# Optimization experiments

Measured on AMD Instinct MI355X. Metric: run time of the kernel, lower is better.

The kernel has to match this reference:

```python
import jax, jax.numpy as jnp
import numpy as np
import math

D_MODEL = 2048
NUM_HEADS = 32
NUM_KV_HEADS = 8
HEAD_DIM = D_MODEL // NUM_HEADS  # 64
BATCH = 2
SEQ = 2048


def setup_inputs() -> dict:
    key = jax.random.key(0)
    ks = jax.random.split(key, 5)
    std_q = math.sqrt(2.0 / (D_MODEL + D_MODEL))
    std_kv = math.sqrt(2.0 / (D_MODEL + NUM_KV_HEADS * HEAD_DIM))
    x = jax.random.normal(ks[0], (BATCH, SEQ, D_MODEL), dtype=jnp.float32)
    Wq = jax.random.normal(ks[1], (D_MODEL, D_MODEL), dtype=jnp.float32) * std_q
    Wk = jax.random.normal(ks[2], (NUM_KV_HEADS * HEAD_DIM, D_MODEL), dtype=jnp.float32) * std_kv
    Wv = jax.random.normal(ks[3], (NUM_KV_HEADS * HEAD_DIM, D_MODEL), dtype=jnp.float32) * std_kv
    Wo = jax.random.normal(ks[4], (D_MODEL, D_MODEL), dtype=jnp.float32) * std_q
    return {"x": x, "Wq": Wq, "Wk": Wk, "Wv": Wv, "Wo": Wo}


def reference(x, Wq, Wk, Wv, Wo):
    B, L, _ = x.shape
    group = NUM_HEADS // NUM_KV_HEADS
    # projections: x @ W.T
    q = (x @ Wq.T).reshape(B, L, NUM_HEADS, HEAD_DIM).transpose(0, 2, 1, 3)      # [B,H,L,D]
    k = (x @ Wk.T).reshape(B, L, NUM_KV_HEADS, HEAD_DIM).transpose(0, 2, 1, 3)   # [B,Hkv,L,D]
    v = (x @ Wv.T).reshape(B, L, NUM_KV_HEADS, HEAD_DIM).transpose(0, 2, 1, 3)
    # expand KV heads (repeat_interleave along head dim)
    k = jnp.repeat(k, group, axis=1)  # [B,H,L,D]
    v = jnp.repeat(v, group, axis=1)
    scale = 1.0 / math.sqrt(HEAD_DIM)
    scores = jnp.einsum("bhld,bhsd->bhls", q, k) * scale  # [B,H,L,S]
    causal_mask = jnp.tril(jnp.ones((L, L), dtype=bool))
    scores = jnp.where(causal_mask[None, None], scores, -jnp.inf)
    weights = jax.nn.softmax(scores, axis=-1)
    out = jnp.einsum("bhls,bhsd->bhld", weights, v)  # [B,H,L,D]
    out = out.transpose(0, 2, 1, 3).reshape(B, L, D_MODEL)
    return out @ Wo.T
```

## Files before the change

### kernel.cpp

```cpp
#include <hip/hip_runtime.h>
#include <stdint.h>


typedef unsigned short u16;
typedef short bf16x8 __attribute__((ext_vector_type(8)));
typedef float f32x4 __attribute__((ext_vector_type(4)));

#define D_MODEL 2048
#define QKV_DIM 3072
#define NUM_HEADS 32
#define HEAD_DIM 64
#define SEQ 2048
#define MTOT 4096

static __device__ __forceinline__ u16 f2bf(float f){
  uint32_t u = __builtin_bit_cast(uint32_t, f);
  u += 0x7FFFu + ((u >> 16) & 1u);
  return (u16)(u >> 16);
}

static __device__ __forceinline__ float exp2_fast(float x){
  float r;
  asm("v_exp_f32 %0, %1" : "=v"(r) : "v"(x));
  return r;
}

static __device__ __forceinline__ uint32_t cvt_pk_bf16(float lo, float hi){
  uint32_t r;
  asm("v_cvt_pk_bf16_f32 %0, %1, %2" : "=v"(r) : "v"(lo), "v"(hi));
  return r;
}

static __device__ __forceinline__ void gload16(const u16* g, u16* l){
  __builtin_amdgcn_global_load_lds(
      (__attribute__((address_space(1))) uint32_t*)(uintptr_t)g,
      (__attribute__((address_space(3))) uint32_t*)l,
      16, 0, 0);
}

__global__ __launch_bounds__(256)
void cvt_bf16(const float* __restrict__ in, u16* __restrict__ out, int n,
              float scl){
  const int i = (blockIdx.x * 256 + threadIdx.x) * 8;
  if (i >= n) return;
  float4 a = *(const float4*)(in + i);
  float4 b = *(const float4*)(in + i + 4);
  union { u16 h[8]; uint4 v; } t;
  t.h[0]=f2bf(a.x*scl); t.h[1]=f2bf(a.y*scl); t.h[2]=f2bf(a.z*scl); t.h[3]=f2bf(a.w*scl);
  t.h[4]=f2bf(b.x*scl); t.h[5]=f2bf(b.y*scl); t.h[6]=f2bf(b.z*scl); t.h[7]=f2bf(b.w*scl);
  *(uint4*)(out + i) = t.v;
}

template <bool F32OUT>
__global__ __launch_bounds__(256)
void gemm_bt(const u16* __restrict__ A, const u16* __restrict__ B,
             void* __restrict__ Cv, int M, int N, int K){
  constexpr int BK = 32;
  __shared__ __attribute__((aligned(16))) u16 As[128*BK];
  __shared__ __attribute__((aligned(16))) u16 Bs[128*BK];
  const int tid  = threadIdx.x;
  const int wave = tid >> 6, lane = tid & 63;
  const int quad = lane >> 4, l16 = lane & 15;
  const int wrow = wave >> 1, wcol = wave & 1;
  const int m0 = blockIdx.y * 128, n0 = blockIdx.x * 128;
  const int srow = lane >> 2, scol = (lane & 3) * 8;

  const f32x4 zero = {0.f, 0.f, 0.f, 0.f};
  f32x4 acc[4][4];
#pragma unroll
  for (int i = 0; i < 4; i++)
#pragma unroll
    for (int j = 0; j < 4; j++) acc[i][j] = zero;

  for (int k0 = 0; k0 < K; k0 += BK){
#pragma unroll
    for (int t = 0; t < 2; t++){
      const int chunk = wave + t*4;
      gload16(A + (size_t)(m0 + chunk*16 + srow)*K + k0 + scol, As + chunk*16*BK);
      gload16(B + (size_t)(n0 + chunk*16 + srow)*K + k0 + scol, Bs + chunk*16*BK);
    }
    __syncthreads();
    bf16x8 af[4], bfr[4];
#pragma unroll
    for (int mi = 0; mi < 4; mi++)
      af[mi] = *(const bf16x8*)(As + (wrow*64 + mi*16 + l16)*BK + quad*8);
#pragma unroll
    for (int ni = 0; ni < 4; ni++)
      bfr[ni] = *(const bf16x8*)(Bs + (wcol*64 + ni*16 + l16)*BK + quad*8);
#pragma unroll
    for (int mi = 0; mi < 4; mi++)
#pragma unroll
      for (int ni = 0; ni < 4; ni++)
        acc[mi][ni] = __builtin_amdgcn_mfma_f32_16x16x32_bf16(af[mi], bfr[ni], acc[mi][ni], 0, 0, 0);
    __syncthreads();
  }
#pragma unroll
  for (int mi = 0; mi < 4; mi++)
#pragma unroll
    for (int ni = 0; ni < 4; ni++){
      const int col = n0 + wcol*64 + ni*16 + l16;
#pragma unroll
      for (int r = 0; r < 4; r++){
        const int row = m0 + wrow*64 + mi*16 + quad*4 + r;
        if constexpr (F32OUT)
          ((float*)Cv)[(size_t)row*N + col] = acc[mi][ni][r];
        else
          ((u16*)Cv)[(size_t)row*N + col] = f2bf(acc[mi][ni][r]);
      }
    }
}

__global__ __launch_bounds__(256)
void kvtrans(const u16* __restrict__ QKV, u16* __restrict__ Ksw,
             u16* __restrict__ Vsw){
  __shared__ u16 Ls[64*72];
  const int tid = threadIdx.x;
  const int st = blockIdx.x, hk = blockIdx.y, b = blockIdx.z;
  const size_t rb = (size_t)b * SEQ;
  const size_t tbase = ((size_t)(b*8 + hk)*32 + st) * 4096;

#pragma unroll
  for (int t = 0; t < 2; t++){
    const int task = t*256 + tid;
    const int r = task >> 3, c = task & 7;
    uint4 kv = *(const uint4*)(QKV + (rb + st*64 + r)*QKV_DIM + 2048 + hk*HEAD_DIM + c*8);
    *(uint4*)(Ksw + tbase + r*64 + (size_t)((c ^ (r & 7)) * 8)) = kv;
  }
#pragma unroll
  for (int t = 0; t < 2; t++){
    const int task = t*256 + tid;
    const int r = task >> 3, c = task & 7;
    *(uint4*)(Ls + r*72 + c*8) =
        *(const uint4*)(QKV + (rb + st*64 + r)*QKV_DIM + 2560 + hk*HEAD_DIM + c*8);
  }
  __syncthreads();
#pragma unroll
  for (int t = 0; t < 2; t++){
    const int task = t*256 + tid;
    const int d = task >> 3, sc = task & 7;
    union { u16 h[8]; uint4 v; } tmp;
#pragma unroll
    for (int e = 0; e < 8; e++){
      const int key = ((2*(sc>>2) + (e>>2))<<4) + ((sc&3)<<2) + (e&3);
      tmp.h[e] = Ls[key*72 + d];
    }
    *(uint4*)(Vsw + tbase + d*64 + (size_t)((sc ^ (d & 7)) * 8)) = tmp.v;
  }
}

__global__ __launch_bounds__(256)
void attn(const u16* __restrict__ Q, const u16* __restrict__ Ksw,
          const u16* __restrict__ Vsw, u16* __restrict__ O, int qs){
  __shared__ __attribute__((aligned(16))) u16 Ks[64*64];
  __shared__ __attribute__((aligned(16))) u16 Vt[64*64];
  const int tid = threadIdx.x;
  const int wave = tid >> 6, lane = tid & 63, quad = lane >> 4, l16 = lane & 15;
  const int g_ = (blockIdx.x + blockIdx.y) & 31;
  const int qt = blockIdx.z ? (31 - g_) : g_;
  const int h = blockIdx.y, b = blockIdx.z;
  const int hk = h >> 2;
  const size_t rb = (size_t)b * SEQ;
  const size_t hb = ((size_t)(b*8 + hk)) * 32;

  const int qrow = wave*16 + l16;
  const int sw = l16 & 7;

  bf16x8 qf[2];
  {
    const u16* qp = Q + (rb + qt*64 + wave*16 + l16)*qs + h*HEAD_DIM;
    qf[0] = *(const bf16x8*)(qp + quad*8);
    qf[1] = *(const bf16x8*)(qp + 32 + quad*8);
  }
  const f32x4 zero = {0.f, 0.f, 0.f, 0.f};
  f32x4 oacc[4];
#pragma unroll
  for (int i = 0; i < 4; i++) oacc[i] = zero;
  float m_i = -INFINITY;
  float l_i = 0.f;

  for (int j = 0; j <= qt; ++j){
    {
      const u16* kt = Ksw + (hb + j) * 4096;
      const u16* vt = Vsw + (hb + j) * 4096;
#pragma unroll
      for (int t = 0; t < 2; t++){
        const int ch = wave*2 + t;
        gload16(kt + ch*512 + lane*8, Ks + ch*512);
        gload16(vt + ch*512 + lane*8, Vt + ch*512);
      }
    }
    __syncthreads();

    f32x4 st[4];
#pragma unroll
    for (int ni = 0; ni < 4; ni++){
      f32x4 s = zero;
#pragma unroll
      for (int ss = 0; ss < 2; ss++){
        bf16x8 kf = *(const bf16x8*)(Ks + ((ni*16 + l16) << 6) +
                                     (((ss*4 + quad) ^ sw) << 3));
        s = __builtin_amdgcn_mfma_f32_16x16x32_bf16(kf, qf[ss], s, 0, 0, 0);
      }
      st[ni] = s;
    }
    if (j == qt){
#pragma unroll
      for (int ni = 0; ni < 4; ni++)
#pragma unroll
        for (int r = 0; r < 4; r++)
          if (ni*16 + quad*4 + r > qrow) st[ni][r] = -INFINITY;
    }

    float mx = fmaxf(fmaxf(fmaxf(st[0][0], st[0][1]), fmaxf(st[0][2], st[0][3])),
                     fmaxf(fmaxf(st[1][0], st[1][1]), fmaxf(st[1][2], st[1][3])));
    mx = fmaxf(mx, fmaxf(fmaxf(fmaxf(st[2][0], st[2][1]), fmaxf(st[2][2], st[2][3])),
                         fmaxf(fmaxf(st[3][0], st[3][1]), fmaxf(st[3][2], st[3][3]))));
    mx = fmaxf(mx, __shfl_xor(mx, 16));
    mx = fmaxf(mx, __shfl_xor(mx, 32));

    if (__all(mx <= m_i + 10.f)){
      float ps = 0.f;
#pragma unroll
      for (int ni = 0; ni < 4; ni++)
#pragma unroll
        for (int r = 0; r < 4; r++){
          const float p = exp2_fast(st[ni][r] - m_i);
          st[ni][r] = p;
          ps += p;
        }
      ps += __shfl_xor(ps, 16);
      ps += __shfl_xor(ps, 32);
      l_i += ps;
    } else {
      const float mn = fmaxf(m_i, mx);
      const float alpha = exp2_fast(m_i - mn);
      float ps = 0.f;
#pragma unroll
      for (int ni = 0; ni < 4; ni++)
#pragma unroll
        for (int r = 0; r < 4; r++){
          const float p = exp2_fast(st[ni][r] - mn);
          st[ni][r] = p;
          ps += p;
        }
      ps += __shfl_xor(ps, 16);
      ps += __shfl_xor(ps, 32);
      l_i = l_i*alpha + ps;
      m_i = mn;
      float ar[4];
#pragma unroll
      for (int r = 0; r < 4; r++) ar[r] = __shfl(alpha, quad*4 + r);
#pragma unroll
      for (int ci = 0; ci < 4; ci++)
#pragma unroll
        for (int r = 0; r < 4; r++) oacc[ci][r] *= ar[r];
    }

    bf16x8 pfr[2];
#pragma unroll
    for (int ss = 0; ss < 2; ss++){
      union { uint32_t w[4]; bf16x8 v; } pk;
      pk.w[0] = cvt_pk_bf16(st[2*ss][0],   st[2*ss][1]);
      pk.w[1] = cvt_pk_bf16(st[2*ss][2],   st[2*ss][3]);
      pk.w[2] = cvt_pk_bf16(st[2*ss+1][0], st[2*ss+1][1]);
      pk.w[3] = cvt_pk_bf16(st[2*ss+1][2], st[2*ss+1][3]);
      pfr[ss] = pk.v;
    }

#pragma unroll
    for (int ss = 0; ss < 2; ss++)
#pragma unroll
      for (int ci = 0; ci < 4; ci++){
        bf16x8 vf = *(const bf16x8*)(Vt + ((ci*16 + l16) << 6) +
                                     (((ss*4 + quad) ^ sw) << 3));
        oacc[ci] = __builtin_amdgcn_mfma_f32_16x16x32_bf16(pfr[ss], vf, oacc[ci], 0, 0, 0);
      }
    __syncthreads();
  }

  float lf[4];
#pragma unroll
  for (int r = 0; r < 4; r++) lf[r] = __shfl(l_i, quad*4 + r);
#pragma unroll
  for (int ci = 0; ci < 4; ci++)
#pragma unroll
    for (int r = 0; r < 4; r++){
      const size_t row = rb + qt*64 + wave*16 + quad*4 + r;
      O[row*D_MODEL + h*HEAD_DIM + ci*16 + l16] = f2bf(oacc[ci][r] / lf[r]);
    }
}

extern "C" void kernel_launch(void* const* d_in, const int* in_sizes, int n_in,
                              void* d_out, int out_size, void* d_ws, size_t ws_size,
                              hipStream_t stream){
  const float* x  = (const float*)d_in[0];
  const float* Wq = (const float*)d_in[1];
  const float* Wk = (const float*)d_in[2];
  const float* Wv = (const float*)d_in[3];
  const float* Wo = (const float*)d_in[4];
  float* out = (float*)d_out;

  u16* xb   = (u16*)d_ws;
  u16* Wb   = xb + (size_t)MTOT*D_MODEL;
  u16* QKVb = (u16*)d_out;
  u16* Kswz = Wb;
  u16* Vswz = Wb + (size_t)2*1024*1024;

  const int nx  = MTOT*D_MODEL;
  const int nwq = D_MODEL*D_MODEL;
  const int nwk = 512*D_MODEL;
  const float QSCL = 0.125f * 1.44269504f;

  cvt_bf16<<<nx/2048, 256, 0, stream>>>(x, xb, nx, 1.0f);
  cvt_bf16<<<nwq/2048, 256, 0, stream>>>(Wq, Wb, nwq, QSCL);
  cvt_bf16<<<nwk/2048, 256, 0, stream>>>(Wk, Wb + (size_t)D_MODEL*D_MODEL, nwk, 1.0f);
  cvt_bf16<<<nwk/2048, 256, 0, stream>>>(Wv, Wb + (size_t)2560*D_MODEL, nwk, 1.0f);
  gemm_bt<false><<<dim3(QKV_DIM/128, MTOT/128), 256, 0, stream>>>(xb, Wb, QKVb, MTOT, QKV_DIM, D_MODEL);
  kvtrans<<<dim3(SEQ/64, 8, 2), 256, 0, stream>>>(QKVb, Kswz, Vswz);
  attn<<<dim3(SEQ/64, NUM_HEADS, 2), 256, 0, stream>>>(
      QKVb, Kswz, Vswz, xb, QKV_DIM);
  cvt_bf16<<<nwq/2048, 256, 0, stream>>>(Wo, Wb, nwq, 1.0f);
  gemm_bt<true><<<dim3(D_MODEL/128, MTOT/128), 256, 0, stream>>>(xb, Wb, (void*)out, MTOT, D_MODEL, D_MODEL);
}
```

Baseline: 343.2 us.

## Double-buffer K/V tiles in attention to prefetch next block during compute

The attention kernel now keeps two LDS buffers each for K and V. It issues the global-to-LDS loads for tile j+1 before computing on tile j, and uses a single barrier per iteration instead of two. This is meant to hide global memory latency behind the MFMA and softmax work. In exchange, shared memory per block doubles, which may reduce how many blocks fit on a CU.

```diff
diff --git a/kernel.cpp b/kernel.cpp
--- a/kernel.cpp
+++ b/kernel.cpp
@@ -151,8 +151,8 @@
 __global__ __launch_bounds__(256)
 void attn(const u16* __restrict__ Q, const u16* __restrict__ Ksw,
           const u16* __restrict__ Vsw, u16* __restrict__ O, int qs){
-  __shared__ __attribute__((aligned(16))) u16 Ks[64*64];
-  __shared__ __attribute__((aligned(16))) u16 Vt[64*64];
+  __shared__ __attribute__((aligned(16))) u16 Ks[2][64*64];
+  __shared__ __attribute__((aligned(16))) u16 Vt[2][64*64];
   const int tid = threadIdx.x;
   const int wave = tid >> 6, lane = tid & 63, quad = lane >> 4, l16 = lane & 15;
   const int g_ = (blockIdx.x + blockIdx.y) & 31;
@@ -178,18 +178,32 @@
   float m_i = -INFINITY;
   float l_i = 0.f;
 
+  {
+    const u16* kt = Ksw + hb * 4096;
+    const u16* vt = Vsw + hb * 4096;
+#pragma unroll
+    for (int t = 0; t < 2; t++){
+      const int ch = wave*2 + t;
+      gload16(kt + ch*512 + lane*8, &Ks[0][ch*512]);
+      gload16(vt + ch*512 + lane*8, &Vt[0][ch*512]);
+    }
+  }
+  int cur = 0;
+
   for (int j = 0; j <= qt; ++j){
-    {
-      const u16* kt = Ksw + (hb + j) * 4096;
-      const u16* vt = Vsw + (hb + j) * 4096;
+    __syncthreads();
+    if (j < qt){
+      const u16* kt = Ksw + (hb + j + 1) * 4096;
+      const u16* vt = Vsw + (hb + j + 1) * 4096;
 #pragma unroll
       for (int t = 0; t < 2; t++){
         const int ch = wave*2 + t;
-        gload16(kt + ch*512 + lane*8, Ks + ch*512);
-        gload16(vt + ch*512 + lane*8, Vt + ch*512);
+        gload16(kt + ch*512 + lane*8, &Ks[cur^1][ch*512]);
+        gload16(vt + ch*512 + lane*8, &Vt[cur^1][ch*512]);
       }
     }
-    __syncthreads();
+    const u16* Ksb = Ks[cur];
+    const u16* Vtb = Vt[cur];
 
     f32x4 st[4];
 #pragma unroll
@@ -197,7 +211,7 @@
       f32x4 s = zero;
 #pragma unroll
       for (int ss = 0; ss < 2; ss++){
-        bf16x8 kf = *(const bf16x8*)(Ks + ((ni*16 + l16) << 6) +
+        bf16x8 kf = *(const bf16x8*)(Ksb + ((ni*16 + l16) << 6) +
                                      (((ss*4 + quad) ^ sw) << 3));
         s = __builtin_amdgcn_mfma_f32_16x16x32_bf16(kf, qf[ss], s, 0, 0, 0);
       }
@@ -271,11 +285,11 @@
     for (int ss = 0; ss < 2; ss++)
 #pragma unroll
       for (int ci = 0; ci < 4; ci++){
-        bf16x8 vf = *(const bf16x8*)(Vt + ((ci*16 + l16) << 6) +
+        bf16x8 vf = *(const bf16x8*)(Vtb + ((ci*16 + l16) << 6) +
                                      (((ss*4 + quad) ^ sw) << 3));
         oacc[ci] = __builtin_amdgcn_mfma_f32_16x16x32_bf16(pfr[ss], vf, oacc[ci], 0, 0, 0);
       }
-    __syncthreads();
+    cur ^= 1;
   }
 
   float lf[4];
```

Measured after the change: 341.4 us. Within noise of the previous version (-0.5%).
